# Optimization experiments

Hardware: AMD Instinct MI355X
Metric: run time of the kernel (lower is better)

## Reference

```python
import jax, jax.numpy as jnp
import numpy as np

N_NODES = 50000
N_EDGES = 200000
D = 384
R = 2  # num_relations


def setup_inputs() -> dict:
    key = jax.random.key(0)
    ks = jax.random.split(key, 16)
    inp = {
        "embeddings": jax.random.normal(ks[0], (N_NODES, D), dtype=jnp.float32),
        "edge_index": jax.random.randint(ks[1], (2, N_EDGES), 0, N_NODES, dtype=jnp.int64),
        "edge_type": jax.random.randint(ks[2], (N_EDGES,), 0, R, dtype=jnp.int64),
    }
    # RGCNConv params for 3 layers: per-relation weight, root weight, bias
    s = 1.0 / np.sqrt(D)
    for i, kk in zip((1, 2, 3), range(3)):
        inp[f"W{i}"] = jax.random.uniform(ks[3 + 3 * kk], (R, D, D), dtype=jnp.float32, minval=-s, maxval=s)
        inp[f"root{i}"] = jax.random.uniform(ks[4 + 3 * kk], (D, D), dtype=jnp.float32, minval=-s, maxval=s)
        inp[f"bias{i}"] = jnp.zeros((D,), dtype=jnp.float32)
    return inp


def _rgcn_conv(x, src, dst, edge_type, W, root, bias):
    # PyG RGCNConv with aggr='mean': for each relation, mean-aggregate neighbor
    # features over edges of that relation, then apply relation weight; plus
    # root transform and bias. We transform-then-aggregate (equivalent, linear).
    out = x @ root + bias
    for r in range(R):
        xr = x @ W[r]                                   # [N, D]
        mask = (edge_type == r).astype(x.dtype)         # [E]
        msg = xr[src] * mask[:, None]                   # [E, D] gather
        s = jax.ops.segment_sum(msg, dst, num_segments=N_NODES)    # [N, D]
        cnt = jax.ops.segment_sum(mask, dst, num_segments=N_NODES)  # [N]
        out = out + s / jnp.maximum(cnt, 1.0)[:, None]  # mean (0 if no edges)
    return out


def reference(embeddings, edge_index, edge_type, W1, root1, bias1, W2, root2, bias2, W3, root3, bias3):
    src, dst = edge_index[0], edge_index[1]
    x = jax.nn.relu(_rgcn_conv(embeddings, src, dst, edge_type, W1, root1, bias1))
    # dropout is identity in eval mode
    x = jax.nn.relu(_rgcn_conv(x, src, dst, edge_type, W2, root2, bias2))
    x = _rgcn_conv(x, src, dst, edge_type, W3, root3, bias3)
    return x
```

## Files before the change

### kernel.cpp

```cpp
#include <hip/hip_runtime.h>
#include <hip/hip_bf16.h>


#define D 384
#define NC 1152
#define BM 128
#define BN 128
#define BK 64
#define NTILES 9

typedef __attribute__((ext_vector_type(8))) short short8;
typedef __attribute__((ext_vector_type(4))) float floatx4;
typedef unsigned int uint;
typedef unsigned short ushort;

__device__ __forceinline__ void load_lds16(const void* g, void* l) {
    __builtin_amdgcn_global_load_lds(
        (const __attribute__((address_space(1))) void*)g,
        (__attribute__((address_space(3))) void*)l, 16, 0, 0);
}

__device__ __forceinline__ ushort f2bf(float x) {
    __hip_bfloat16 h = __float2bfloat16(x);
    return *reinterpret_cast<ushort*>(&h);
}

__device__ __forceinline__ uint pack2(float a, float b) {
    return (uint)f2bf(a) | ((uint)f2bf(b) << 16);
}

__global__ __launch_bounds__(256) void gemm_bf16_mfma(
    const ushort* __restrict__ A, const ushort* __restrict__ BT,
    ushort* __restrict__ C, int M)
{
    __shared__ alignas(16) ushort As[BM * BK];
    __shared__ alignas(16) ushort Bs[BN * BK];

    const int b = blockIdx.x;
    const int xcd = b & 7;
    const int t = b >> 3;
    const int bnt = t % NTILES;
    const int bmt = (t / NTILES) * 8 + xcd;
    const int Mtiles = (M + BM - 1) / BM;
    if (bmt >= Mtiles) return;
    const int bm = bmt * BM;
    const int bn = bnt * BN;

    const int tid = threadIdx.x;
    const int wave = tid >> 6;
    const int lane = tid & 63;
    const int wr = wave >> 1;
    const int wc = wave & 1;
    const int l15 = lane & 15;
    const int k8 = lane >> 4;

    floatx4 acc[4][4] = {};

    for (int k0 = 0; k0 < D; k0 += BK) {
        __syncthreads();
#pragma unroll
        for (int j = 0; j < 4; ++j) {
            const int chunk = j * 256 + wave * 64 + lane;
            const int row = chunk >> 3;
            const int cs = chunk & 7;
            const int gc = cs ^ (row & 7);
            const int ga = min(bm + row, M - 1);
            load_lds16(A + (size_t)ga * D + k0 + gc * 8, As + (size_t)chunk * 8);
            load_lds16(BT + (size_t)(bn + row) * D + k0 + gc * 8, Bs + (size_t)chunk * 8);
        }
        __syncthreads();

#pragma unroll
        for (int p = 0; p < 2; ++p) {
            short8 af[4], bfr[4];
            const int kc = p * 4 + k8;
#pragma unroll
            for (int mi = 0; mi < 4; ++mi) {
                const int m = wr * 64 + mi * 16 + l15;
                af[mi] = *(const short8*)(As + m * BK + (kc ^ (m & 7)) * 8);
            }
#pragma unroll
            for (int ni = 0; ni < 4; ++ni) {
                const int n = wc * 64 + ni * 16 + l15;
                bfr[ni] = *(const short8*)(Bs + n * BK + (kc ^ (n & 7)) * 8);
            }
#pragma unroll
            for (int mi = 0; mi < 4; ++mi)
#pragma unroll
                for (int ni = 0; ni < 4; ++ni)
                    acc[mi][ni] = __builtin_amdgcn_mfma_f32_16x16x32_bf16(
                        af[mi], bfr[ni], acc[mi][ni], 0, 0, 0);
        }
    }

#pragma unroll
    for (int mi = 0; mi < 4; ++mi) {
#pragma unroll
        for (int reg = 0; reg < 4; ++reg) {
            const int row = bm + wr * 64 + mi * 16 + k8 * 4 + reg;
            if (row < M) {
#pragma unroll
                for (int ni = 0; ni < 4; ++ni) {
                    const int col = bn + wc * 64 + ni * 16 + l15;
                    C[(size_t)row * NC + col] = f2bf(acc[mi][ni][reg]);
                }
            }
        }
    }
}


__global__ __launch_bounds__(256) void count_edges(
    const int* __restrict__ dst, const int* __restrict__ et,
    int* __restrict__ cntI, int E, int M)
{
    const int e = blockIdx.x * blockDim.x + threadIdx.x;
    if (e < E) atomicAdd(&cntI[(size_t)et[e] * M + dst[e]], 1);
}

__global__ __launch_bounds__(256) void finalize_cnt(
    const int* __restrict__ cntI, float* __restrict__ invc, int n)
{
    const int i = blockIdx.x * blockDim.x + threadIdx.x;
    if (i < n) invc[i] = 1.0f / (float)max(cntI[i], 1);
}

__global__ __launch_bounds__(1024) void scan_local(
    const int* __restrict__ hist, int* __restrict__ offs,
    int* __restrict__ bsums, int n)
{
    __shared__ int tmp[1024];
    const int tid = threadIdx.x;
    const int i = blockIdx.x * 1024 + tid;
    const int v = (i < n) ? hist[i] : 0;
    tmp[tid] = v;
    __syncthreads();
#pragma unroll
    for (int off = 1; off < 1024; off <<= 1) {
        const int add = (tid >= off) ? tmp[tid - off] : 0;
        __syncthreads();
        tmp[tid] += add;
        __syncthreads();
    }
    if (i < n) offs[i] = tmp[tid] - v;
    if (tid == 1023) bsums[blockIdx.x] = tmp[1023];
}

__global__ __launch_bounds__(1024) void scan_bsums(
    int* __restrict__ bsums, int* __restrict__ total_out, int nb)
{
    __shared__ int tmp[1024];
    const int tid = threadIdx.x;
    const int v = (tid < nb) ? bsums[tid] : 0;
    tmp[tid] = v;
    __syncthreads();
#pragma unroll
    for (int off = 1; off < 1024; off <<= 1) {
        const int add = (tid >= off) ? tmp[tid - off] : 0;
        __syncthreads();
        tmp[tid] += add;
        __syncthreads();
    }
    if (tid < nb) bsums[tid] = tmp[tid] - v;
    if (tid == 1023) *total_out = tmp[1023];
}

__global__ __launch_bounds__(1024) void scan_add(
    int* __restrict__ offs, const int* __restrict__ bsums, int n)
{
    const int i = blockIdx.x * 1024 + threadIdx.x;
    if (i < n) offs[i] += bsums[blockIdx.x];
}

__global__ __launch_bounds__(256) void fill_sorted(
    const int* __restrict__ src, const int* __restrict__ dst,
    const int* __restrict__ et, const int* __restrict__ offs,
    int* __restrict__ cursor, int* __restrict__ sorted, int E, int M)
{
    const int e = blockIdx.x * blockDim.x + threadIdx.x;
    if (e < E) {
        const int key = et[e] * M + dst[e];
        const int pos = offs[key] + atomicAdd(&cursor[key], 1);
        sorted[pos] = src[e];
    }
}

__global__ __launch_bounds__(256) void build_bt(
    const float* __restrict__ root1, const float* __restrict__ W1,
    const float* __restrict__ root2, const float* __restrict__ W2,
    const float* __restrict__ root3, const float* __restrict__ W3,
    ushort* __restrict__ BT)
{
    __shared__ float tile[32][33];
    const int l = blockIdx.z;
    const float* root = (l == 0) ? root1 : (l == 1) ? root2 : root3;
    const float* W    = (l == 0) ? W1    : (l == 1) ? W2    : W3;
    const int kt = blockIdx.x * 32;
    const int nt = blockIdx.y * 32;
    const int tx = threadIdx.x & 31;
    const int ty = threadIdx.x >> 5;
    const float* srcm;
    int noff;
    if (nt < D)          { srcm = root;      noff = 0; }
    else if (nt < 2 * D) { srcm = W;         noff = D; }
    else                 { srcm = W + D * D; noff = 2 * D; }
    const int n = nt - noff + tx;
#pragma unroll
    for (int i = 0; i < 4; ++i) {
        const int k = kt + ty + i * 8;
        tile[ty + i * 8][tx] = srcm[(size_t)k * D + n];
    }
    __syncthreads();
    ushort* dst = BT + (size_t)l * NC * D;
#pragma unroll
    for (int i = 0; i < 4; ++i) {
        const int nn = nt + ty + i * 8;
        const int kk = kt + tx;
        dst[(size_t)nn * D + kk] = f2bf(tile[tx][ty + i * 8]);
    }
}

__global__ __launch_bounds__(256) void cast_f32_to_bf16(
    const float* __restrict__ x, ushort* __restrict__ y, int n4)
{
    const int i = blockIdx.x * blockDim.x + threadIdx.x;
    if (i < n4) {
        const float4 v = ((const float4*)x)[i];
        uint2 o;
        o.x = pack2(v.x, v.y);
        o.y = pack2(v.z, v.w);
        ((uint2*)y)[i] = o;
    }
}

__global__ __launch_bounds__(256) void aggregate_all(
    const ushort* __restrict__ TC, const int* __restrict__ sorted,
    const int* __restrict__ offs, const float* __restrict__ invc,
    const float* __restrict__ bias, ushort* __restrict__ outb,
    float* __restrict__ outf, int M, int relu)
{
    const int wave = threadIdx.x >> 6;
    const int lane = threadIdx.x & 63;
    const int d = blockIdx.x * 4 + wave;
    if (d >= M) return;

    float v[6];
    {
        const uint* rp = (const uint*)(TC + (size_t)d * NC);
#pragma unroll
        for (int p = 0; p < 3; ++p) {
            const uint b = rp[lane + 64 * p];
            const float2 bb = *(const float2*)(bias + (lane + 64 * p) * 2);
            v[2 * p]     = __uint_as_float(b << 16) + bb.x;
            v[2 * p + 1] = __uint_as_float(b & 0xffff0000u) + bb.y;
        }
    }
#pragma unroll
    for (int r = 0; r < 2; ++r) {
        const int key = r * M + d;
        const int beg = offs[key], end = offs[key + 1];
        float g[6] = {0.f, 0.f, 0.f, 0.f, 0.f, 0.f};
        for (int i = beg; i < end; ++i) {
            const int s = sorted[i];
            const uint* tp = (const uint*)(TC + (size_t)s * NC + D + r * D);
#pragma unroll
            for (int p = 0; p < 3; ++p) {
                const uint b = tp[lane + 64 * p];
                g[2 * p]     += __uint_as_float(b << 16);
                g[2 * p + 1] += __uint_as_float(b & 0xffff0000u);
            }
        }
        const float ic = invc[key];
#pragma unroll
        for (int j = 0; j < 6; ++j) v[j] += ic * g[j];
    }
    if (relu) {
#pragma unroll
        for (int j = 0; j < 6; ++j) v[j] = fmaxf(v[j], 0.f);
    }
    if (outb) {
        uint* op = (uint*)(outb + (size_t)d * D);
#pragma unroll
        for (int p = 0; p < 3; ++p) op[lane + 64 * p] = pack2(v[2 * p], v[2 * p + 1]);
    } else {
        float2* op = (float2*)(outf + (size_t)d * D);
#pragma unroll
        for (int p = 0; p < 3; ++p)
            op[lane + 64 * p] = make_float2(v[2 * p], v[2 * p + 1]);
    }
}

extern "C" void kernel_launch(void* const* d_in, const int* in_sizes, int n_in,
                              void* d_out, int out_size, void* d_ws, size_t ws_size,
                              hipStream_t stream)
{
    const float* emb   = (const float*)d_in[0];
    const int*   eidx  = (const int*)d_in[1];
    const int*   et    = (const int*)d_in[2];
    const float* W1    = (const float*)d_in[3];
    const float* root1 = (const float*)d_in[4];
    const float* bias1 = (const float*)d_in[5];
    const float* W2    = (const float*)d_in[6];
    const float* root2 = (const float*)d_in[7];
    const float* bias2 = (const float*)d_in[8];
    const float* W3    = (const float*)d_in[9];
    const float* root3 = (const float*)d_in[10];
    const float* bias3 = (const float*)d_in[11];

    float* out = (float*)d_out;
    const int M = in_sizes[0] / D;
    const int E = in_sizes[1] / 2;
    const int* src  = eidx;
    const int* dstv = eidx + E;

    const int n = 2 * M;
    const int nb = (n + 1023) / 1024;

    char* w = (char*)d_ws;
    ushort* TC = (ushort*)w;          w += (size_t)M * NC * 2;
    ushort* Xb = (ushort*)w;          w += (size_t)M * D * 2;
    ushort* BT = (ushort*)w;          w += (size_t)3 * NC * D * 2;
    float* invcnt = (float*)w;        w += (size_t)n * 4;
    int* cntI = (int*)w;              w += (size_t)n * 4;
    int* offs = (int*)w;              w += ((size_t)n + 1) * 4;
    int* sorted = (int*)w;            w += (size_t)E * 4;
    int* bsums = (int*)w;

    hipMemsetAsync(cntI, 0, (size_t)n * sizeof(int), stream);
    count_edges<<<(E + 255) / 256, 256, 0, stream>>>(dstv, et, cntI, E, M);
    finalize_cnt<<<(n + 255) / 256, 256, 0, stream>>>(cntI, invcnt, n);
    scan_local<<<nb, 1024, 0, stream>>>(cntI, offs, bsums, n);
    scan_bsums<<<1, 1024, 0, stream>>>(bsums, offs + n, nb);
    scan_add<<<nb, 1024, 0, stream>>>(offs, bsums, n);
    hipMemsetAsync(cntI, 0, (size_t)n * sizeof(int), stream);
    fill_sorted<<<(E + 255) / 256, 256, 0, stream>>>(src, dstv, et, offs, cntI, sorted, E, M);

    build_bt<<<dim3(D / 32, NC / 32, 3), 256, 0, stream>>>(root1, W1, root2, W2, root3, W3, BT);
    cast_f32_to_bf16<<<(M * D / 4 + 255) / 256, 256, 0, stream>>>(emb, Xb, M * D / 4);

    const int Mtiles = (M + BM - 1) / BM;
    const int gemm_blocks = 8 * NTILES * ((Mtiles + 7) / 8);
    const float* biases[3] = {bias1, bias2, bias3};
    for (int l = 0; l < 3; ++l) {
        gemm_bf16_mfma<<<gemm_blocks, 256, 0, stream>>>(Xb, BT + (size_t)l * NC * D, TC, M);
        const bool last = (l == 2);
        aggregate_all<<<(M + 3) / 4, 256, 0, stream>>>(
            TC, sorted, offs, invcnt, biases[l],
            last ? nullptr : Xb, last ? out : nullptr, M, last ? 0 : 1);
    }
}
```

Before: 499.2 us.

## Rewrite GEMM as 256x256 tile, 8-wave kernel with 4-stage LDS pipeline

Replaces the 128x128 single-buffered GEMM with a 256x256 tile, 512-thread kernel that uses four LDS stages, manual vmcnt waits and split A/B prefetch interleaved with MFMA phases under raised wave priority. Weights are padded to 1280 columns so the N dimension tiles evenly, and workgroups are remapped contiguously per XCD for L2 locality. The aim is to hide global-to-LDS latency and raise MFMA utilization. The cost is heavier register and LDS use, wasted compute on the padded columns, and fragile hand-written wait counts.

After: 518.6 us. 1.04x slower.

```diff
diff --git a/kernel.cpp b/kernel.cpp
--- a/kernel.cpp
+++ b/kernel.cpp
@@ -4,16 +4,24 @@
 
 #define D 384
 #define NC 1152
-#define BM 128
-#define BN 128
-#define BK 64
-#define NTILES 9
+#define NP 1280
+#define BM 256
+#define BN 256
+#define BK 32
+#define NKT (D / BK)
+#define NTN (NP / BN)
 
 typedef __attribute__((ext_vector_type(8))) short short8;
 typedef __attribute__((ext_vector_type(4))) float floatx4;
 typedef unsigned int uint;
 typedef unsigned short ushort;
 
+#define BAR() asm volatile("s_barrier" ::: "memory")
+#define WAIT_LGKM0() asm volatile("s_waitcnt lgkmcnt(0)" ::: "memory")
+#define WAIT_VM8() asm volatile("s_waitcnt vmcnt(8)" ::: "memory")
+#define WAIT_VM4() asm volatile("s_waitcnt vmcnt(4)" ::: "memory")
+#define WAIT_VM0() asm volatile("s_waitcnt vmcnt(0)" ::: "memory")
+
 __device__ __forceinline__ void load_lds16(const void* g, void* l) {
     __builtin_amdgcn_global_load_lds(
         (const __attribute__((address_space(1))) void*)g,
@@ -29,80 +37,134 @@
     return (uint)f2bf(a) | ((uint)f2bf(b) << 16);
 }
 
-__global__ __launch_bounds__(256) void gemm_bf16_mfma(
+__device__ __forceinline__ void stage_tile(const ushort* __restrict__ g,
+                                           ushort* l, int grow0, int kt,
+                                           int rmax, int tid)
+{
+#pragma unroll
+    for (int j = 0; j < 2; ++j) {
+        const int ch = j * 512 + tid;
+        const int row = ch >> 2;
+        const int cs = ch & 3;
+        const int gc = cs ^ ((row >> 1) & 3);
+        const int gr = min(grow0 + row, rmax);
+        load_lds16(g + (size_t)gr * D + kt * BK + gc * 8, l + (size_t)ch * 8);
+    }
+}
+
+__global__ __launch_bounds__(512, 2) void gemm_bf16_mfma(
     const ushort* __restrict__ A, const ushort* __restrict__ BT,
-    ushort* __restrict__ C, int M)
-{
-    __shared__ alignas(16) ushort As[BM * BK];
-    __shared__ alignas(16) ushort Bs[BN * BK];
-
-    const int b = blockIdx.x;
-    const int xcd = b & 7;
-    const int t = b >> 3;
-    const int bnt = t % NTILES;
-    const int bmt = (t / NTILES) * 8 + xcd;
-    const int Mtiles = (M + BM - 1) / BM;
-    if (bmt >= Mtiles) return;
-    const int bm = bmt * BM;
-    const int bn = bnt * BN;
+    ushort* __restrict__ C, int M, int nwg)
+{
+    __shared__ alignas(16) ushort As[4][BM * BK];
+    __shared__ alignas(16) ushort Bs[4][BN * BK];
+
+    const int o = blockIdx.x;
+    const int xcd = o & 7, lid = o >> 3;
+    const int q = nwg >> 3, r = nwg & 7;
+    const int wg = (xcd < r ? xcd * (q + 1) : r * (q + 1) + (xcd - r) * q) + lid;
+    const int bnt = wg % NTN, bmt = wg / NTN;
+    const int bm = bmt * BM, bn = bnt * BN;
 
     const int tid = threadIdx.x;
-    const int wave = tid >> 6;
-    const int lane = tid & 63;
-    const int wr = wave >> 1;
-    const int wc = wave & 1;
-    const int l15 = lane & 15;
-    const int k8 = lane >> 4;
-
-    floatx4 acc[4][4] = {};
-
-    for (int k0 = 0; k0 < D; k0 += BK) {
-        __syncthreads();
-#pragma unroll
-        for (int j = 0; j < 4; ++j) {
-            const int chunk = j * 256 + wave * 64 + lane;
-            const int row = chunk >> 3;
-            const int cs = chunk & 7;
-            const int gc = cs ^ (row & 7);
-            const int ga = min(bm + row, M - 1);
-            load_lds16(A + (size_t)ga * D + k0 + gc * 8, As + (size_t)chunk * 8);
-            load_lds16(BT + (size_t)(bn + row) * D + k0 + gc * 8, Bs + (size_t)chunk * 8);
-        }
-        __syncthreads();
-
-#pragma unroll
-        for (int p = 0; p < 2; ++p) {
-            short8 af[4], bfr[4];
-            const int kc = p * 4 + k8;
-#pragma unroll
-            for (int mi = 0; mi < 4; ++mi) {
-                const int m = wr * 64 + mi * 16 + l15;
-                af[mi] = *(const short8*)(As + m * BK + (kc ^ (m & 7)) * 8);
-            }
-#pragma unroll
-            for (int ni = 0; ni < 4; ++ni) {
-                const int n = wc * 64 + ni * 16 + l15;
-                bfr[ni] = *(const short8*)(Bs + n * BK + (kc ^ (n & 7)) * 8);
-            }
-#pragma unroll
-            for (int mi = 0; mi < 4; ++mi)
-#pragma unroll
-                for (int ni = 0; ni < 4; ++ni)
-                    acc[mi][ni] = __builtin_amdgcn_mfma_f32_16x16x32_bf16(
-                        af[mi], bfr[ni], acc[mi][ni], 0, 0, 0);
-        }
-    }
-
-#pragma unroll
-    for (int mi = 0; mi < 4; ++mi) {
-#pragma unroll
-        for (int reg = 0; reg < 4; ++reg) {
-            const int row = bm + wr * 64 + mi * 16 + k8 * 4 + reg;
-            if (row < M) {
+    const int wave = tid >> 6, lane = tid & 63;
+    const int wr = wave >> 2, wc = wave & 3;
+    const int l15 = lane & 15, k8 = lane >> 4;
+
+    floatx4 acc[8][4] = {};
+
+    stage_tile(A, As[0], bm, 0, M - 1, tid);
+    stage_tile(BT, Bs[0], bn, 0, NP - 1, tid);
+    stage_tile(A, As[1], bm, 1, M - 1, tid);
+    stage_tile(BT, Bs[1], bn, 1, NP - 1, tid);
+    stage_tile(A, As[2], bm, 2, M - 1, tid);
+    stage_tile(BT, Bs[2], bn, 2, NP - 1, tid);
+    WAIT_VM8();
+    BAR();
+
+    short8 bf[4];
+    for (int j = 0; j < NKT; ++j) {
+        const ushort* Ab = As[j & 3];
+        const ushort* Bb = Bs[j & 3];
+        const int js = j + 3;
+        const int sb = js & 3;
+
+        short8 af[4];
+#pragma unroll
+        for (int mi = 0; mi < 4; ++mi) {
+            const int m = wr * 128 + mi * 16 + l15;
+            af[mi] = *(const short8*)(Ab + m * BK + ((k8 ^ ((m >> 1) & 3)) << 3));
+        }
+#pragma unroll
+        for (int ni = 0; ni < 4; ++ni) {
+            const int n = wc * 64 + ni * 16 + l15;
+            bf[ni] = *(const short8*)(Bb + n * BK + ((k8 ^ ((n >> 1) & 3)) << 3));
+        }
+        if (js < NKT) stage_tile(A, As[sb], bm, js, M - 1, tid);
+        BAR();
+        WAIT_LGKM0();
+        __builtin_amdgcn_sched_barrier(0);
+        __builtin_amdgcn_s_setprio(1);
+#pragma unroll
+        for (int mi = 0; mi < 4; ++mi)
+#pragma unroll
+            for (int ni = 0; ni < 4; ++ni)
+                acc[mi][ni] = __builtin_amdgcn_mfma_f32_16x16x32_bf16(
+                    af[mi], bf[ni], acc[mi][ni], 0, 0, 0);
+        __builtin_amdgcn_s_setprio(0);
+        BAR();
+
+#pragma unroll
+        for (int mi = 0; mi < 4; ++mi) {
+            const int m = wr * 128 + 64 + mi * 16 + l15;
+            af[mi] = *(const short8*)(Ab + m * BK + ((k8 ^ ((m >> 1) & 3)) << 3));
+        }
+        if (js < NKT) stage_tile(BT, Bs[sb], bn, js, NP - 1, tid);
+        BAR();
+        WAIT_LGKM0();
+        __builtin_amdgcn_sched_barrier(0);
+        __builtin_amdgcn_s_setprio(1);
+#pragma unroll
+        for (int mi = 0; mi < 4; ++mi)
+#pragma unroll
+            for (int ni = 0; ni < 4; ++ni)
+                acc[4 + mi][ni] = __builtin_amdgcn_mfma_f32_16x16x32_bf16(
+                    af[mi], bf[ni], acc[4 + mi][ni], 0, 0, 0);
+        __builtin_amdgcn_s_setprio(0);
+        if (j < NKT - 3)       { WAIT_VM8(); }
+        else if (j == NKT - 3) { WAIT_VM4(); }
+        else if (j == NKT - 2) { WAIT_VM0(); }
+        BAR();
+    }
+
+    if (bm + BM <= M && bn + BN <= NC) {
+#pragma unroll
+        for (int a = 0; a < 8; ++a) {
+            const int rbase = bm + wr * 128 + (a >> 2) * 64 + (a & 3) * 16 + k8 * 4;
+#pragma unroll
+            for (int reg = 0; reg < 4; ++reg) {
+                const int row = rbase + reg;
 #pragma unroll
                 for (int ni = 0; ni < 4; ++ni) {
                     const int col = bn + wc * 64 + ni * 16 + l15;
-                    C[(size_t)row * NC + col] = f2bf(acc[mi][ni][reg]);
+                    C[(size_t)row * NC + col] = f2bf(acc[a][ni][reg]);
+                }
+            }
+        }
+    } else {
+#pragma unroll
+        for (int a = 0; a < 8; ++a) {
+            const int rbase = bm + wr * 128 + (a >> 2) * 64 + (a & 3) * 16 + k8 * 4;
+#pragma unroll
+            for (int reg = 0; reg < 4; ++reg) {
+                const int row = rbase + reg;
+                if (row < M) {
+#pragma unroll
+                    for (int ni = 0; ni < 4; ++ni) {
+                        const int col = bn + wc * 64 + ni * 16 + l15;
+                        if (col < NC)
+                            C[(size_t)row * NC + col] = f2bf(acc[a][ni][reg]);
+                    }
                 }
             }
         }
@@ -211,7 +273,7 @@
         tile[ty + i * 8][tx] = srcm[(size_t)k * D + n];
     }
     __syncthreads();
-    ushort* dst = BT + (size_t)l * NC * D;
+    ushort* dst = BT + (size_t)l * NP * D;
 #pragma unroll
     for (int i = 0; i < 4; ++i) {
         const int nn = nt + ty + i * 8;
@@ -319,7 +381,7 @@
     char* w = (char*)d_ws;
     ushort* TC = (ushort*)w;          w += (size_t)M * NC * 2;
     ushort* Xb = (ushort*)w;          w += (size_t)M * D * 2;
-    ushort* BT = (ushort*)w;          w += (size_t)3 * NC * D * 2;
+    ushort* BT = (ushort*)w;          w += (size_t)3 * NP * D * 2;
     float* invcnt = (float*)w;        w += (size_t)n * 4;
     int* cntI = (int*)w;              w += (size_t)n * 4;
     int* offs = (int*)w;              w += ((size_t)n + 1) * 4;
@@ -339,10 +401,10 @@
     cast_f32_to_bf16<<<(M * D / 4 + 255) / 256, 256, 0, stream>>>(emb, Xb, M * D / 4);
 
     const int Mtiles = (M + BM - 1) / BM;
-    const int gemm_blocks = 8 * NTILES * ((Mtiles + 7) / 8);
+    const int nwg = Mtiles * NTN;
     const float* biases[3] = {bias1, bias2, bias3};
     for (int l = 0; l < 3; ++l) {
-        gemm_bf16_mfma<<<gemm_blocks, 256, 0, stream>>>(Xb, BT + (size_t)l * NC * D, TC, M);
+        gemm_bf16_mfma<<<nwg, 512, 0, stream>>>(Xb, BT + (size_t)l * NP * D, TC, M, nwg);
         const bool last = (l == 2);
         aggregate_all<<<(M + 3) / 4, 256, 0, stream>>>(
             TC, sorted, offs, invcnt, biases[l],
```
